# Optimization experiments

Measured on AMD Instinct MI355X. Metric: run time of the kernel, lower is better.

## Reference

```python
import jax, jax.numpy as jnp
import numpy as np

B = 256
NUM_CAPS = 2            # digit capsules
N_IN = 6 * 6 * 6 * 32   # 6912 input capsules
D_OUT = 16
D_IN = 8
N_ROUTING = 3           # original loops range(3 - 1) = 2 iterations
EPS = 1e-9


def squash(s):
    # squash along last axis: (|s|^2/(1+|s|^2)) * s/|s|
    n2 = jnp.sum(s * s, axis=-1, keepdims=True)
    return (n2 / (1.0 + n2)) * s / jnp.sqrt(n2 + EPS)


def setup_inputs() -> dict:
    key = jax.random.key(0)
    k1, k2 = jax.random.split(key)
    x = jax.random.normal(k1, (B, N_IN, D_IN), dtype=jnp.float32)
    W = jax.random.normal(k2, (NUM_CAPS, N_IN, D_OUT, D_IN), dtype=jnp.float32) * 0.1
    return {"x": x, "W": W}


def reference(x, W):
    # tile x over the 2 digit capsules + per-(capsule, input-capsule) matvec:
    # u_hat[b,j,n,e] = sum_d W[j,n,e,d] * x[b,n,d]   -> [B, 2, N, 16]
    u_hat = jnp.einsum('bnd,jned->bjne', x, W)
    b_logits = jnp.zeros(u_hat.shape[:3], dtype=x.dtype)  # [B, 2, N]
    v = None
    for _ in range(N_ROUTING - 1):
        c = jax.nn.softmax(b_logits, axis=1)               # softmax over the 2 capsules (dim=1 in source)
        s = jnp.einsum('bjn,bjne->bje', c, u_hat)          # [B, 2, 16]
        v = squash(s)
        b_logits = b_logits + jnp.einsum('bje,bjne->bjn', v, u_hat)
    return v
```

## Files before the change

### kernel.cpp

```cpp
#include <hip/hip_runtime.h>

#define B_ 256
#define J_ 2
#define N_ 6912
#define E_ 16
#define D_ 8
#define NB 36
#define CGX 192
#define BSTR (4*N_*D_)

__device__ __forceinline__ float dpp_row_add16(float v){
  v += __int_as_float(__builtin_amdgcn_update_dpp(0, __float_as_int(v), 0xB1,  0xF, 0xF, true));
  v += __int_as_float(__builtin_amdgcn_update_dpp(0, __float_as_int(v), 0x4E,  0xF, 0xF, true));
  v += __int_as_float(__builtin_amdgcn_update_dpp(0, __float_as_int(v), 0x141, 0xF, 0xF, true));
  v += __int_as_float(__builtin_amdgcn_update_dpp(0, __float_as_int(v), 0x140, 0xF, 0xF, true));
  return v;
}


__global__ __launch_bounds__(256, 3) void kpass1(const float* __restrict__ x,
                                                 const float* __restrict__ W,
                                                 float* __restrict__ partial)
{
  __shared__ float smem[9216];
  const int tid  = threadIdx.x;
  const int lane = tid & 63;
  const int wv   = __builtin_amdgcn_readfirstlane(tid >> 6);
  const int e    = lane & 15;
  const int blo  = lane >> 4;
  const int nb0  = blockIdx.x * NB;

  float4 wbuf[9];
  #pragma unroll
  for (int k=0;k<9;++k){
    const int idx = k*256 + tid;
    const int j   = (idx >= 1152) ? 1 : 0;
    const int r4  = idx - j*1152;
    wbuf[k] = *(const float4*)(W + ((size_t)j*N_ + nb0)*(E_*D_) + (size_t)r4*4);
  }
  #pragma unroll
  for (int k=0;k<9;++k)
    *(float4*)(smem + (size_t)(k*256 + tid)*4) = wbuf[k];

  const int b0 = blockIdx.y*64 + wv*16 + blo;
  const float* xp = x + ((size_t)b0*N_ + nb0)*D_;

  float4 xa[4], xb[4];
  #pragma unroll
  for (int k=0;k<4;++k){
    xa[k] = *(const float4*)(xp + (size_t)k*BSTR);
    xb[k] = *(const float4*)(xp + (size_t)k*BSTR + 4);
  }
  __syncthreads();

  float acc0[4] = {0,0,0,0}, acc1[4] = {0,0,0,0};
  #pragma unroll 1
  for (int ni=0; ni<NB; ++ni){
    float4 ca[4], cb[4];
    #pragma unroll
    for (int k=0;k<4;++k){ ca[k]=xa[k]; cb[k]=xb[k]; }
    if (ni+1 < NB){
      #pragma unroll
      for (int k=0;k<4;++k){
        xa[k] = *(const float4*)(xp + (size_t)k*BSTR + (ni+1)*8);
        xb[k] = *(const float4*)(xp + (size_t)k*BSTR + (ni+1)*8 + 4);
      }
    }
    const float* wp0 = smem + ni*(E_*D_) + e*8;
    const float4 wa0 = *(const float4*)(wp0);
    const float4 wb0 = *(const float4*)(wp0 + 4);
    const float4 wa1 = *(const float4*)(wp0 + NB*(E_*D_));
    const float4 wb1 = *(const float4*)(wp0 + NB*(E_*D_) + 4);
    #pragma unroll
    for (int k=0;k<4;++k){
      float a0 = acc0[k], a1 = acc1[k];
      a0 = fmaf(wa0.x, ca[k].x, a0); a0 = fmaf(wa0.y, ca[k].y, a0);
      a0 = fmaf(wa0.z, ca[k].z, a0); a0 = fmaf(wa0.w, ca[k].w, a0);
      a0 = fmaf(wb0.x, cb[k].x, a0); a0 = fmaf(wb0.y, cb[k].y, a0);
      a0 = fmaf(wb0.z, cb[k].z, a0); a0 = fmaf(wb0.w, cb[k].w, a0);
      a1 = fmaf(wa1.x, ca[k].x, a1); a1 = fmaf(wa1.y, ca[k].y, a1);
      a1 = fmaf(wa1.z, ca[k].z, a1); a1 = fmaf(wa1.w, ca[k].w, a1);
      a1 = fmaf(wb1.x, cb[k].x, a1); a1 = fmaf(wb1.y, cb[k].y, a1);
      a1 = fmaf(wb1.z, cb[k].z, a1); a1 = fmaf(wb1.w, cb[k].w, a1);
      acc0[k] = a0; acc1[k] = a1;
    }
  }

  float* dst = partial + (size_t)(blockIdx.x*4 + blockIdx.y)*2048
             + (wv*16 + blo)*32 + e;
  #pragma unroll
  for (int k=0;k<4;++k){
    dst[k*128]      = acc0[k];
    dst[k*128 + 16] = acc1[k];
  }
}

__global__ __launch_bounds__(256, 3) void kpass2(const float* __restrict__ x,
                                                 const float* __restrict__ W,
                                                 const float* __restrict__ v1,
                                                 float* __restrict__ partial)
{
  __shared__ float smem[9216];
  const int tid  = threadIdx.x;
  const int lane = tid & 63;
  const int wv   = __builtin_amdgcn_readfirstlane(tid >> 6);
  const int e    = lane & 15;
  const int blo  = lane >> 4;
  const int nb0  = blockIdx.x * NB;

  float4 wbuf[9];
  #pragma unroll
  for (int k=0;k<9;++k){
    const int idx = k*256 + tid;
    const int j   = (idx >= 1152) ? 1 : 0;
    const int r4  = idx - j*1152;
    wbuf[k] = *(const float4*)(W + ((size_t)j*N_ + nb0)*(E_*D_) + (size_t)r4*4);
  }
  #pragma unroll
  for (int k=0;k<9;++k)
    *(float4*)(smem + (size_t)(k*256 + tid)*4) = wbuf[k];

  const int b0 = blockIdx.y*64 + wv*16 + blo;
  const float* xp = x + ((size_t)b0*N_ + nb0)*D_;

  float4 xa[4], xb[4];
  #pragma unroll
  for (int k=0;k<4;++k){
    xa[k] = *(const float4*)(xp + (size_t)k*BSTR);
    xb[k] = *(const float4*)(xp + (size_t)k*BSTR + 4);
  }
  float vj0[4], vj1[4];
  #pragma unroll
  for (int k=0;k<4;++k){
    vj0[k] = v1[(size_t)(b0 + 4*k)*32 + e];
    vj1[k] = v1[(size_t)(b0 + 4*k)*32 + 16 + e];
  }
  __syncthreads();

  float acc0[4] = {0,0,0,0}, acc1[4] = {0,0,0,0};
  #pragma unroll 1
  for (int ni=0; ni<NB; ++ni){
    float4 ca[4], cb[4];
    #pragma unroll
    for (int k=0;k<4;++k){ ca[k]=xa[k]; cb[k]=xb[k]; }
    if (ni+1 < NB){
      #pragma unroll
      for (int k=0;k<4;++k){
        xa[k] = *(const float4*)(xp + (size_t)k*BSTR + (ni+1)*8);
        xb[k] = *(const float4*)(xp + (size_t)k*BSTR + (ni+1)*8 + 4);
      }
    }
    const float* wp0 = smem + ni*(E_*D_) + e*8;
    const float4 wa0 = *(const float4*)(wp0);
    const float4 wb0 = *(const float4*)(wp0 + 4);
    const float4 wa1 = *(const float4*)(wp0 + NB*(E_*D_));
    const float4 wb1 = *(const float4*)(wp0 + NB*(E_*D_) + 4);

    float u0[4], u1[4];
    #pragma unroll
    for (int k=0;k<4;++k){
      float a0, a1;
      a0 = wa0.x*ca[k].x;        a0 = fmaf(wa0.y, ca[k].y, a0);
      a0 = fmaf(wa0.z, ca[k].z, a0); a0 = fmaf(wa0.w, ca[k].w, a0);
      a0 = fmaf(wb0.x, cb[k].x, a0); a0 = fmaf(wb0.y, cb[k].y, a0);
      a0 = fmaf(wb0.z, cb[k].z, a0); a0 = fmaf(wb0.w, cb[k].w, a0);
      a1 = wa1.x*ca[k].x;        a1 = fmaf(wa1.y, ca[k].y, a1);
      a1 = fmaf(wa1.z, ca[k].z, a1); a1 = fmaf(wa1.w, ca[k].w, a1);
      a1 = fmaf(wb1.x, cb[k].x, a1); a1 = fmaf(wb1.y, cb[k].y, a1);
      a1 = fmaf(wb1.z, cb[k].z, a1); a1 = fmaf(wb1.w, cb[k].w, a1);
      u0[k] = a0; u1[k] = a1;
    }
    #pragma unroll
    for (int k=0;k<4;++k){
      const float d  = dpp_row_add16(fmaf(vj1[k], u1[k], -(vj0[k]*u0[k])));
      const float c0 = __builtin_amdgcn_rcpf(1.f + __expf(d));
      acc0[k] = fmaf(c0,       u0[k], acc0[k]);
      acc1[k] = fmaf(1.f - c0, u1[k], acc1[k]);
    }
  }

  float* dst = partial + (size_t)(blockIdx.x*4 + blockIdx.y)*2048
             + (wv*16 + blo)*32 + e;
  #pragma unroll
  for (int k=0;k<4;++k){
    dst[k*128]      = acc0[k];
    dst[k*128 + 16] = acc1[k];
  }
}

template<bool HALF>
__global__ __launch_bounds__(256) void kred(const float* __restrict__ partial,
                                            float* __restrict__ dst)
{
  const int t = blockIdx.x*256 + threadIdx.x;
  const int btile = t >> 11, q = t & 2047;
  const float* p = partial + (size_t)btile*2048 + q;
  float s = 0.f;
  #pragma unroll 8
  for (int cx=0; cx<CGX; ++cx) s += p[(size_t)cx*8192];
  if (HALF) s *= 0.5f;
  float n2 = s*s;
  #pragma unroll
  for (int m=1; m<16; m<<=1) n2 += __shfl_xor(n2, m);
  const float f = (n2/(1.f+n2)) * rsqrtf(n2 + 1e-9f);
  dst[t] = s * f;
}

#define NT 512
__global__ __launch_bounds__(NT) void kmono(const float* __restrict__ x,
                                            const float* __restrict__ W,
                                            float* __restrict__ out)
{
  const int b    = blockIdx.x;
  const int tid  = threadIdx.x;
  const int wv   = tid >> 6;
  const int lane = tid & 63;
  __shared__ float wred[8*33];
  __shared__ float vsh[32];

  float acc[32];
  #pragma unroll
  for (int i=0;i<32;++i) acc[i]=0.f;
  for (int n = tid; n < N_; n += NT){
    const float4 xa = *(const float4*)(x + ((size_t)b*N_ + n)*D_);
    const float4 xb = *(const float4*)(x + ((size_t)b*N_ + n)*D_ + 4);
    #pragma unroll
    for (int j=0;j<J_;++j){
      const float* wp = W + ((size_t)j*N_ + n)*(E_*D_);
      #pragma unroll
      for (int e=0;e<E_;++e){
        const float4 wa = *(const float4*)(wp + e*8);
        const float4 wb = *(const float4*)(wp + e*8 + 4);
        float a = acc[j*16+e];
        a = fmaf(wa.x,xa.x,a); a = fmaf(wa.y,xa.y,a); a = fmaf(wa.z,xa.z,a); a = fmaf(wa.w,xa.w,a);
        a = fmaf(wb.x,xb.x,a); a = fmaf(wb.y,xb.y,a); a = fmaf(wb.z,xb.z,a); a = fmaf(wb.w,xb.w,a);
        acc[j*16+e] = a;
      }
    }
  }
  #pragma unroll
  for (int i=0;i<32;++i){
    float v = acc[i];
    #pragma unroll
    for (int off=32; off; off>>=1) v += __shfl_xor(v, off);
    acc[i] = v;
  }
  if (lane == 0){
    #pragma unroll
    for (int i=0;i<32;++i) wred[wv*33 + i] = acc[i];
  }
  __syncthreads();
  if (tid < 32){
    float s = 0.f;
    #pragma unroll
    for (int w=0;w<8;++w) s += wred[w*33 + tid];
    wred[tid] = 0.5f * s;
  }
  __syncthreads();
  if (tid < 32){
    const int j = tid >> 4; float n2 = 0.f;
    #pragma unroll
    for (int e=0;e<16;++e){ const float sv = wred[j*16+e]; n2 = fmaf(sv,sv,n2); }
    vsh[tid] = wred[tid] * (n2/(1.f+n2)) * rsqrtf(n2 + 1e-9f);
  }
  __syncthreads();
  float vv[32];
  #pragma unroll
  for (int i=0;i<32;++i) vv[i] = vsh[i];

  #pragma unroll
  for (int i=0;i<32;++i) acc[i]=0.f;
  for (int n = tid; n < N_; n += NT){
    const float4 xa = *(const float4*)(x + ((size_t)b*N_ + n)*D_);
    const float4 xb = *(const float4*)(x + ((size_t)b*N_ + n)*D_ + 4);
    float u[32];
    #pragma unroll
    for (int j=0;j<J_;++j){
      const float* wp = W + ((size_t)j*N_ + n)*(E_*D_);
      #pragma unroll
      for (int e=0;e<E_;++e){
        const float4 wa = *(const float4*)(wp + e*8);
        const float4 wb = *(const float4*)(wp + e*8 + 4);
        float a;
        a = wa.x*xa.x; a = fmaf(wa.y,xa.y,a); a = fmaf(wa.z,xa.z,a); a = fmaf(wa.w,xa.w,a);
        a = fmaf(wb.x,xb.x,a); a = fmaf(wb.y,xb.y,a); a = fmaf(wb.z,xb.z,a); a = fmaf(wb.w,xb.w,a);
        u[j*16+e] = a;
      }
    }
    float l0=0.f, l1=0.f;
    #pragma unroll
    for (int e=0;e<16;++e){ l0 = fmaf(vv[e],u[e],l0); l1 = fmaf(vv[16+e],u[16+e],l1); }
    const float c0 = 1.f/(1.f + __expf(l1 - l0));
    const float c1 = 1.f - c0;
    #pragma unroll
    for (int e=0;e<16;++e){ acc[e] = fmaf(c0,u[e],acc[e]); acc[16+e] = fmaf(c1,u[16+e],acc[16+e]); }
  }
  #pragma unroll
  for (int i=0;i<32;++i){
    float v = acc[i];
    #pragma unroll
    for (int off=32; off; off>>=1) v += __shfl_xor(v, off);
    acc[i] = v;
  }
  __syncthreads();
  if (lane == 0){
    #pragma unroll
    for (int i=0;i<32;++i) wred[wv*33 + i] = acc[i];
  }
  __syncthreads();
  if (tid < 32){
    float s = 0.f;
    #pragma unroll
    for (int w=0;w<8;++w) s += wred[w*33 + tid];
    wred[tid] = s;
  }
  __syncthreads();
  if (tid < 32){
    const int j = tid >> 4; float n2 = 0.f;
    #pragma unroll
    for (int e=0;e<16;++e){ const float sv = wred[j*16+e]; n2 = fmaf(sv,sv,n2); }
    out[(size_t)b*32 + tid] = wred[tid] * (n2/(1.f+n2)) * rsqrtf(n2 + 1e-9f);
  }
}

extern "C" void kernel_launch(void* const* d_in, const int* in_sizes, int n_in,
                              void* d_out, int out_size, void* d_ws, size_t ws_size,
                              hipStream_t stream)
{
  const float* x = (const float*)d_in[0];
  const float* W = (const float*)d_in[1];
  if (n_in >= 2 && in_sizes[0] < in_sizes[1]){
    x = (const float*)d_in[1]; W = (const float*)d_in[0];
  }
  float* out = (float*)d_out;

  const size_t need_main = (size_t)(8192 + 768*2048) * sizeof(float);

  if (ws_size >= need_main){
    float* wsf     = (float*)d_ws;
    float* v1      = wsf;
    float* partial = wsf + 8192;
    kpass1<<<dim3(CGX,4), 256, 0, stream>>>(x, W, partial);
    kred<true ><<<32, 256, 0, stream>>>(partial, v1);
    kpass2<<<dim3(CGX,4), 256, 0, stream>>>(x, W, v1, partial);
    kred<false><<<32, 256, 0, stream>>>(partial, out);
  } else {
    kmono<<<B_, NT, 0, stream>>>(x, W, out);
  }
}
```

Baseline: 170.5 us.

## Retile capsule passes to 27-capsule blocks with swizzled LDS and double-buffered x loads

Templates the two routing passes on the per-block capsule count and occupancy, launching 256x4 blocks of 27 input capsules with min 4 waves per SIMD when the workspace is large enough. W is stored in LDS with an XOR swizzle to cut bank conflicts on the per-lane float4 reads. x loads are software-pipelined with two register buffers in a manually unrolled-by-2 loop. Smaller LDS tiles raise occupancy but produce more partials for the reduction kernel to sum, and need a larger workspace.

After: 197.2 us. +15.7%, slower.

```diff
diff --git a/kernel.cpp b/kernel.cpp
--- a/kernel.cpp
+++ b/kernel.cpp
@@ -5,8 +5,6 @@
 #define N_ 6912
 #define E_ 16
 #define D_ 8
-#define NB 36
-#define CGX 192
 #define BSTR (4*N_*D_)
 
 __device__ __forceinline__ float dpp_row_add16(float v){
@@ -17,74 +15,139 @@
   return v;
 }
 
-
-__global__ __launch_bounds__(256, 3) void kpass1(const float* __restrict__ x,
-                                                 const float* __restrict__ W,
-                                                 float* __restrict__ partial)
-{
-  __shared__ float smem[9216];
+__device__ __forceinline__ void ldx(const float* __restrict__ xp, int ni,
+                                    float4 (&xa)[4], float4 (&xb)[4]){
+  #pragma unroll
+  for (int k=0;k<4;++k){
+    xa[k] = *(const float4*)(xp + (size_t)k*BSTR + ni*8);
+    xb[k] = *(const float4*)(xp + (size_t)k*BSTR + ni*8 + 4);
+  }
+}
+
+template<int NBT>
+__device__ __forceinline__ void body1(const float4* __restrict__ smem4, int ni,
+                                      int sA, int sB,
+                                      const float4 (&xa)[4], const float4 (&xb)[4],
+                                      float (&acc0)[4], float (&acc1)[4]){
+  const float4 wa0 = smem4[ni*32 + sA];
+  const float4 wb0 = smem4[ni*32 + sB];
+  const float4 wa1 = smem4[(NBT + ni)*32 + sA];
+  const float4 wb1 = smem4[(NBT + ni)*32 + sB];
+  #pragma unroll
+  for (int k=0;k<4;++k){
+    float a0 = acc0[k], a1 = acc1[k];
+    a0 = fmaf(wa0.x, xa[k].x, a0); a0 = fmaf(wa0.y, xa[k].y, a0);
+    a0 = fmaf(wa0.z, xa[k].z, a0); a0 = fmaf(wa0.w, xa[k].w, a0);
+    a0 = fmaf(wb0.x, xb[k].x, a0); a0 = fmaf(wb0.y, xb[k].y, a0);
+    a0 = fmaf(wb0.z, xb[k].z, a0); a0 = fmaf(wb0.w, xb[k].w, a0);
+    a1 = fmaf(wa1.x, xa[k].x, a1); a1 = fmaf(wa1.y, xa[k].y, a1);
+    a1 = fmaf(wa1.z, xa[k].z, a1); a1 = fmaf(wa1.w, xa[k].w, a1);
+    a1 = fmaf(wb1.x, xb[k].x, a1); a1 = fmaf(wb1.y, xb[k].y, a1);
+    a1 = fmaf(wb1.z, xb[k].z, a1); a1 = fmaf(wb1.w, xb[k].w, a1);
+    acc0[k] = a0; acc1[k] = a1;
+  }
+}
+
+template<int NBT>
+__device__ __forceinline__ void body2(const float4* __restrict__ smem4, int ni,
+                                      int sA, int sB,
+                                      const float4 (&xa)[4], const float4 (&xb)[4],
+                                      const float (&vj0)[4], const float (&vj1)[4],
+                                      float (&acc0)[4], float (&acc1)[4]){
+  const float4 wa0 = smem4[ni*32 + sA];
+  const float4 wb0 = smem4[ni*32 + sB];
+  const float4 wa1 = smem4[(NBT + ni)*32 + sA];
+  const float4 wb1 = smem4[(NBT + ni)*32 + sB];
+  float u0[4], u1[4];
+  #pragma unroll
+  for (int k=0;k<4;++k){
+    float a0, a1;
+    a0 = wa0.x*xa[k].x;            a0 = fmaf(wa0.y, xa[k].y, a0);
+    a0 = fmaf(wa0.z, xa[k].z, a0); a0 = fmaf(wa0.w, xa[k].w, a0);
+    a0 = fmaf(wb0.x, xb[k].x, a0); a0 = fmaf(wb0.y, xb[k].y, a0);
+    a0 = fmaf(wb0.z, xb[k].z, a0); a0 = fmaf(wb0.w, xb[k].w, a0);
+    a1 = wa1.x*xa[k].x;            a1 = fmaf(wa1.y, xa[k].y, a1);
+    a1 = fmaf(wa1.z, xa[k].z, a1); a1 = fmaf(wa1.w, xa[k].w, a1);
+    a1 = fmaf(wb1.x, xb[k].x, a1); a1 = fmaf(wb1.y, xb[k].y, a1);
+    a1 = fmaf(wb1.z, xb[k].z, a1); a1 = fmaf(wb1.w, xb[k].w, a1);
+    u0[k] = a0; u1[k] = a1;
+  }
+  #pragma unroll
+  for (int k=0;k<4;++k){
+    const float d  = dpp_row_add16(fmaf(vj1[k], u1[k], -(vj0[k]*u0[k])));
+    const float c0 = __builtin_amdgcn_rcpf(1.f + __expf(d));
+    acc0[k] = fmaf(c0,       u0[k], acc0[k]);
+    acc1[k] = fmaf(1.f - c0, u1[k], acc1[k]);
+  }
+}
+
+template<int NBT>
+__device__ __forceinline__ void stageW(const float* __restrict__ W, int nb0, int tid,
+                                       float4* __restrict__ smem4, float4 (&wbuf)[(J_*NBT*32 + 255)/256]){
+  constexpr int TOT4 = J_*NBT*32;
+  constexpr int KS = (TOT4 + 255)/256;
+  #pragma unroll
+  for (int k=0;k<KS;++k){
+    const int idx = k*256 + tid;
+    if (TOT4 % 256 == 0 || idx < TOT4){
+      const int j  = (idx >= NBT*32) ? 1 : 0;
+      const int r4 = idx - j*(NBT*32);
+      wbuf[k] = *(const float4*)(W + ((size_t)j*N_ + nb0)*(E_*D_) + (size_t)r4*4);
+    }
+  }
+}
+
+template<int NBT>
+__device__ __forceinline__ void writeW(int tid, float4* __restrict__ smem4,
+                                       const float4 (&wbuf)[(J_*NBT*32 + 255)/256]){
+  constexpr int TOT4 = J_*NBT*32;
+  constexpr int KS = (TOT4 + 255)/256;
+  #pragma unroll
+  for (int k=0;k<KS;++k){
+    const int idx = k*256 + tid;
+    if (TOT4 % 256 == 0 || idx < TOT4){
+      const int u = idx & 31;
+      smem4[(idx & ~31) | (u ^ (u>>3))] = wbuf[k];
+    }
+  }
+}
+
+
+template<int NBT, int MINW>
+__global__ __launch_bounds__(256, MINW) void kpass1(const float* __restrict__ x,
+                                                    const float* __restrict__ W,
+                                                    float* __restrict__ partial)
+{
+  __shared__ float4 smem4[J_*NBT*32];
   const int tid  = threadIdx.x;
   const int lane = tid & 63;
   const int wv   = __builtin_amdgcn_readfirstlane(tid >> 6);
   const int e    = lane & 15;
   const int blo  = lane >> 4;
-  const int nb0  = blockIdx.x * NB;
-
-  float4 wbuf[9];
-  #pragma unroll
-  for (int k=0;k<9;++k){
-    const int idx = k*256 + tid;
-    const int j   = (idx >= 1152) ? 1 : 0;
-    const int r4  = idx - j*1152;
-    wbuf[k] = *(const float4*)(W + ((size_t)j*N_ + nb0)*(E_*D_) + (size_t)r4*4);
-  }
-  #pragma unroll
-  for (int k=0;k<9;++k)
-    *(float4*)(smem + (size_t)(k*256 + tid)*4) = wbuf[k];
+  const int nb0  = blockIdx.x * NBT;
+
+  float4 wbuf[(J_*NBT*32 + 255)/256];
+  stageW<NBT>(W, nb0, tid, smem4, wbuf);
 
   const int b0 = blockIdx.y*64 + wv*16 + blo;
   const float* xp = x + ((size_t)b0*N_ + nb0)*D_;
-
-  float4 xa[4], xb[4];
-  #pragma unroll
-  for (int k=0;k<4;++k){
-    xa[k] = *(const float4*)(xp + (size_t)k*BSTR);
-    xb[k] = *(const float4*)(xp + (size_t)k*BSTR + 4);
-  }
+  const int sA = (e*2)   ^ ((e*2)>>3);
+  const int sB = (e*2+1) ^ ((e*2+1)>>3);
+
+  float4 xaA[4], xbA[4], xaB[4], xbB[4];
+  ldx(xp, 0, xaA, xbA);
+  writeW<NBT>(tid, smem4, wbuf);
   __syncthreads();
 
   float acc0[4] = {0,0,0,0}, acc1[4] = {0,0,0,0};
   #pragma unroll 1
-  for (int ni=0; ni<NB; ++ni){
-    float4 ca[4], cb[4];
-    #pragma unroll
-    for (int k=0;k<4;++k){ ca[k]=xa[k]; cb[k]=xb[k]; }
-    if (ni+1 < NB){
-      #pragma unroll
-      for (int k=0;k<4;++k){
-        xa[k] = *(const float4*)(xp + (size_t)k*BSTR + (ni+1)*8);
-        xb[k] = *(const float4*)(xp + (size_t)k*BSTR + (ni+1)*8 + 4);
-      }
-    }
-    const float* wp0 = smem + ni*(E_*D_) + e*8;
-    const float4 wa0 = *(const float4*)(wp0);
-    const float4 wb0 = *(const float4*)(wp0 + 4);
-    const float4 wa1 = *(const float4*)(wp0 + NB*(E_*D_));
-    const float4 wb1 = *(const float4*)(wp0 + NB*(E_*D_) + 4);
-    #pragma unroll
-    for (int k=0;k<4;++k){
-      float a0 = acc0[k], a1 = acc1[k];
-      a0 = fmaf(wa0.x, ca[k].x, a0); a0 = fmaf(wa0.y, ca[k].y, a0);
-      a0 = fmaf(wa0.z, ca[k].z, a0); a0 = fmaf(wa0.w, ca[k].w, a0);
-      a0 = fmaf(wb0.x, cb[k].x, a0); a0 = fmaf(wb0.y, cb[k].y, a0);
-      a0 = fmaf(wb0.z, cb[k].z, a0); a0 = fmaf(wb0.w, cb[k].w, a0);
-      a1 = fmaf(wa1.x, ca[k].x, a1); a1 = fmaf(wa1.y, ca[k].y, a1);
-      a1 = fmaf(wa1.z, ca[k].z, a1); a1 = fmaf(wa1.w, ca[k].w, a1);
-      a1 = fmaf(wb1.x, cb[k].x, a1); a1 = fmaf(wb1.y, cb[k].y, a1);
-      a1 = fmaf(wb1.z, cb[k].z, a1); a1 = fmaf(wb1.w, cb[k].w, a1);
-      acc0[k] = a0; acc1[k] = a1;
-    }
-  }
+  for (int ni=0; ni+1<NBT; ni+=2){
+    ldx(xp, ni+1, xaB, xbB);
+    body1<NBT>(smem4, ni, sA, sB, xaA, xbA, acc0, acc1);
+    if (ni+2 < NBT) ldx(xp, ni+2, xaA, xbA);
+    body1<NBT>(smem4, ni+1, sA, sB, xaB, xbB, acc0, acc1);
+  }
+  if (NBT & 1) body1<NBT>(smem4, NBT-1, sA, sB, xaA, xbA, acc0, acc1);
 
   float* dst = partial + (size_t)(blockIdx.x*4 + blockIdx.y)*2048
              + (wv*16 + blo)*32 + e;
@@ -95,89 +158,48 @@
   }
 }
 
-__global__ __launch_bounds__(256, 3) void kpass2(const float* __restrict__ x,
-                                                 const float* __restrict__ W,
-                                                 const float* __restrict__ v1,
-                                                 float* __restrict__ partial)
-{
-  __shared__ float smem[9216];
+template<int NBT, int MINW>
+__global__ __launch_bounds__(256, MINW) void kpass2(const float* __restrict__ x,
+                                                    const float* __restrict__ W,
+                                                    const float* __restrict__ v1,
+                                                    float* __restrict__ partial)
+{
+  __shared__ float4 smem4[J_*NBT*32];
   const int tid  = threadIdx.x;
   const int lane = tid & 63;
   const int wv   = __builtin_amdgcn_readfirstlane(tid >> 6);
   const int e    = lane & 15;
   const int blo  = lane >> 4;
-  const int nb0  = blockIdx.x * NB;
-
-  float4 wbuf[9];
-  #pragma unroll
-  for (int k=0;k<9;++k){
-    const int idx = k*256 + tid;
-    const int j   = (idx >= 1152) ? 1 : 0;
-    const int r4  = idx - j*1152;
-    wbuf[k] = *(const float4*)(W + ((size_t)j*N_ + nb0)*(E_*D_) + (size_t)r4*4);
-  }
-  #pragma unroll
-  for (int k=0;k<9;++k)
-    *(float4*)(smem + (size_t)(k*256 + tid)*4) = wbuf[k];
+  const int nb0  = blockIdx.x * NBT;
+
+  float4 wbuf[(J_*NBT*32 + 255)/256];
+  stageW<NBT>(W, nb0, tid, smem4, wbuf);
 
   const int b0 = blockIdx.y*64 + wv*16 + blo;
   const float* xp = x + ((size_t)b0*N_ + nb0)*D_;
-
-  float4 xa[4], xb[4];
-  #pragma unroll
-  for (int k=0;k<4;++k){
-    xa[k] = *(const float4*)(xp + (size_t)k*BSTR);
-    xb[k] = *(const float4*)(xp + (size_t)k*BSTR + 4);
-  }
+  const int sA = (e*2)   ^ ((e*2)>>3);
+  const int sB = (e*2+1) ^ ((e*2+1)>>3);
+
+  float4 xaA[4], xbA[4], xaB[4], xbB[4];
+  ldx(xp, 0, xaA, xbA);
   float vj0[4], vj1[4];
   #pragma unroll
   for (int k=0;k<4;++k){
     vj0[k] = v1[(size_t)(b0 + 4*k)*32 + e];
     vj1[k] = v1[(size_t)(b0 + 4*k)*32 + 16 + e];
   }
+  writeW<NBT>(tid, smem4, wbuf);
   __syncthreads();
 
   float acc0[4] = {0,0,0,0}, acc1[4] = {0,0,0,0};
   #pragma unroll 1
-  for (int ni=0; ni<NB; ++ni){
-    float4 ca[4], cb[4];
-    #pragma unroll
-    for (int k=0;k<4;++k){ ca[k]=xa[k]; cb[k]=xb[k]; }
-    if (ni+1 < NB){
-      #pragma unroll
-      for (int k=0;k<4;++k){
-        xa[k] = *(const float4*)(xp + (size_t)k*BSTR + (ni+1)*8);
-        xb[k] = *(const float4*)(xp + (size_t)k*BSTR + (ni+1)*8 + 4);
-      }
-    }
-    const float* wp0 = smem + ni*(E_*D_) + e*8;
-    const float4 wa0 = *(const float4*)(wp0);
-    const float4 wb0 = *(const float4*)(wp0 + 4);
-    const float4 wa1 = *(const float4*)(wp0 + NB*(E_*D_));
-    const float4 wb1 = *(const float4*)(wp0 + NB*(E_*D_) + 4);
-
-    float u0[4], u1[4];
-    #pragma unroll
-    for (int k=0;k<4;++k){
-      float a0, a1;
-      a0 = wa0.x*ca[k].x;        a0 = fmaf(wa0.y, ca[k].y, a0);
-      a0 = fmaf(wa0.z, ca[k].z, a0); a0 = fmaf(wa0.w, ca[k].w, a0);
-      a0 = fmaf(wb0.x, cb[k].x, a0); a0 = fmaf(wb0.y, cb[k].y, a0);
-      a0 = fmaf(wb0.z, cb[k].z, a0); a0 = fmaf(wb0.w, cb[k].w, a0);
-      a1 = wa1.x*ca[k].x;        a1 = fmaf(wa1.y, ca[k].y, a1);
-      a1 = fmaf(wa1.z, ca[k].z, a1); a1 = fmaf(wa1.w, ca[k].w, a1);
-      a1 = fmaf(wb1.x, cb[k].x, a1); a1 = fmaf(wb1.y, cb[k].y, a1);
-      a1 = fmaf(wb1.z, cb[k].z, a1); a1 = fmaf(wb1.w, cb[k].w, a1);
-      u0[k] = a0; u1[k] = a1;
-    }
-    #pragma unroll
-    for (int k=0;k<4;++k){
-      const float d  = dpp_row_add16(fmaf(vj1[k], u1[k], -(vj0[k]*u0[k])));
-      const float c0 = __builtin_amdgcn_rcpf(1.f + __expf(d));
-      acc0[k] = fmaf(c0,       u0[k], acc0[k]);
-      acc1[k] = fmaf(1.f - c0, u1[k], acc1[k]);
-    }
-  }
+  for (int ni=0; ni+1<NBT; ni+=2){
+    ldx(xp, ni+1, xaB, xbB);
+    body2<NBT>(smem4, ni, sA, sB, xaA, xbA, vj0, vj1, acc0, acc1);
+    if (ni+2 < NBT) ldx(xp, ni+2, xaA, xbA);
+    body2<NBT>(smem4, ni+1, sA, sB, xaB, xbB, vj0, vj1, acc0, acc1);
+  }
+  if (NBT & 1) body2<NBT>(smem4, NBT-1, sA, sB, xaA, xbA, vj0, vj1, acc0, acc1);
 
   float* dst = partial + (size_t)(blockIdx.x*4 + blockIdx.y)*2048
              + (wv*16 + blo)*32 + e;
@@ -188,7 +210,7 @@
   }
 }
 
-template<bool HALF>
+template<bool HALF, int CGXN>
 __global__ __launch_bounds__(256) void kred(const float* __restrict__ partial,
                                             float* __restrict__ dst)
 {
@@ -197,7 +219,7 @@
   const float* p = partial + (size_t)btile*2048 + q;
   float s = 0.f;
   #pragma unroll 8
-  for (int cx=0; cx<CGX; ++cx) s += p[(size_t)cx*8192];
+  for (int cx=0; cx<CGXN; ++cx) s += p[(size_t)cx*8192];
   if (HALF) s *= 0.5f;
   float n2 = s*s;
   #pragma unroll
@@ -334,16 +356,25 @@
   }
   float* out = (float*)d_out;
 
-  const size_t need_main = (size_t)(8192 + 768*2048) * sizeof(float);
-
-  if (ws_size >= need_main){
+  const size_t need_big  = (size_t)(8192 + 1024*2048) * sizeof(float);
+  const size_t need_main = (size_t)(8192 +  768*2048) * sizeof(float);
+
+  if (ws_size >= need_big){
     float* wsf     = (float*)d_ws;
     float* v1      = wsf;
     float* partial = wsf + 8192;
-    kpass1<<<dim3(CGX,4), 256, 0, stream>>>(x, W, partial);
-    kred<true ><<<32, 256, 0, stream>>>(partial, v1);
-    kpass2<<<dim3(CGX,4), 256, 0, stream>>>(x, W, v1, partial);
-    kred<false><<<32, 256, 0, stream>>>(partial, out);
+    kpass1<27,4><<<dim3(256,4), 256, 0, stream>>>(x, W, partial);
+    kred<true ,256><<<32, 256, 0, stream>>>(partial, v1);
+    kpass2<27,4><<<dim3(256,4), 256, 0, stream>>>(x, W, v1, partial);
+    kred<false,256><<<32, 256, 0, stream>>>(partial, out);
+  } else if (ws_size >= need_main){
+    float* wsf     = (float*)d_ws;
+    float* v1      = wsf;
+    float* partial = wsf + 8192;
+    kpass1<36,3><<<dim3(192,4), 256, 0, stream>>>(x, W, partial);
+    kred<true ,192><<<32, 256, 0, stream>>>(partial, v1);
+    kpass2<36,3><<<dim3(192,4), 256, 0, stream>>>(x, W, v1, partial);
+    kred<false,192><<<32, 256, 0, stream>>>(partial, out);
   } else {
     kmono<<<B_, NT, 0, stream>>>(x, W, out);
   }
```
